# Performance work log

Measured on AMD Instinct MI355X. Metric: run time of the kernel, lower is better.

The kernel has to match this reference:

```python
import jax, jax.numpy as jnp
import numpy as np

N = 100000      # nodes
E = 1600000     # directed edges (before self-loops)
DIN = 128       # input feature dim
HID = 32        # per-head hidden dim
HEADS = 4
D1 = HID * HEADS  # 128, concat width
NG = 64         # graphs in batch
NEG_SLOPE = 0.2 # PyG GATConv leaky_relu slope


def setup_inputs() -> dict:
    key = jax.random.key(0)
    ks = jax.random.split(key, 16)
    s = 0.05
    x = jax.random.normal(ks[0], (N, DIN), dtype=jnp.float32)
    edge_index = jax.random.randint(ks[1], (2, E), 0, N, dtype=jnp.int32)
    batch = jnp.sort(jax.random.randint(ks[2], (N,), 0, NG, dtype=jnp.int32))
    # GATConv 1: in=DIN, out=HID, heads=HEADS, concat=True
    W1 = jax.random.normal(ks[3], (D1, DIN), dtype=jnp.float32) * s
    a1s = jax.random.normal(ks[4], (HEADS, HID), dtype=jnp.float32) * s
    a1d = jax.random.normal(ks[5], (HEADS, HID), dtype=jnp.float32) * s
    b1 = jnp.zeros((D1,), jnp.float32)
    # GATConv 2: in=D1, out=HID, heads=HEADS, concat=True
    W2 = jax.random.normal(ks[6], (D1, D1), dtype=jnp.float32) * s
    a2s = jax.random.normal(ks[7], (HEADS, HID), dtype=jnp.float32) * s
    a2d = jax.random.normal(ks[8], (HEADS, HID), dtype=jnp.float32) * s
    b2 = jnp.zeros((D1,), jnp.float32)
    # GATConv 3: in=D1, out=HID, heads=HEADS, concat=False (mean over heads)
    W3 = jax.random.normal(ks[9], (D1, D1), dtype=jnp.float32) * s
    a3s = jax.random.normal(ks[10], (HEADS, HID), dtype=jnp.float32) * s
    a3d = jax.random.normal(ks[11], (HEADS, HID), dtype=jnp.float32) * s
    b3 = jnp.zeros((HID,), jnp.float32)
    lin_w = jax.random.normal(ks[12], (1, HID), dtype=jnp.float32) * s
    lin_b = jnp.zeros((1,), jnp.float32)
    return {"x": x, "edge_index": edge_index, "batch": batch,
            "W1": W1, "a1s": a1s, "a1d": a1d, "b1": b1,
            "W2": W2, "a2s": a2s, "a2d": a2d, "b2": b2,
            "W3": W3, "a3s": a3s, "a3d": a3d, "b3": b3,
            "lin_w": lin_w, "lin_b": lin_b}


def _gat_conv(x, ei, W, att_src, att_dst, bias, concat):
    """PyG GATConv (no edge features, self-loops already in ei)."""
    n = x.shape[0]
    h = (x @ W.T).reshape(n, HEADS, HID)          # [N, H, C]
    src, dst = ei[0], ei[1]
    a_src = jnp.einsum('nhc,hc->nh', h, att_src)  # [N, H]
    a_dst = jnp.einsum('nhc,hc->nh', h, att_dst)
    e = jax.nn.leaky_relu(a_src[src] + a_dst[dst], NEG_SLOPE)  # [Etot, H]
    # segment softmax over incoming edges of each dst node
    e_max = jax.ops.segment_max(e, dst, num_segments=n)
    ex = jnp.exp(e - e_max[dst])
    denom = jax.ops.segment_sum(ex, dst, num_segments=n)
    alpha = ex / denom[dst]                        # [Etot, H]
    out = jax.ops.segment_sum(h[src] * alpha[:, :, None], dst, num_segments=n)
    if concat:
        out = out.reshape(n, HEADS * HID)
    else:
        out = out.mean(axis=1)
    return out + bias


def reference(x, edge_index, batch, W1, a1s, a1d, b1, W2, a2s, a2d, b2,
              W3, a3s, a3d, b3, lin_w, lin_b):
    loops = jnp.arange(N, dtype=edge_index.dtype)
    ei = jnp.concatenate([edge_index, jnp.stack([loops, loops])], axis=1)
    h = jax.nn.elu(_gat_conv(x, ei, W1, a1s, a1d, b1, True))
    h = jax.nn.elu(_gat_conv(h, ei, W2, a2s, a2d, b2, True))
    h = jax.nn.elu(_gat_conv(h, ei, W3, a3s, a3d, b3, False))
    h = h @ lin_w.T + lin_b                        # [N, 1]
    counts = jax.ops.segment_sum(jnp.ones((N,), h.dtype), batch, num_segments=NG)
    pooled = jax.ops.segment_sum(h, batch, num_segments=NG) / counts[:, None]
    return pooled.squeeze()                        # [NG]
```

## Files before the change

### kernel.cpp

```cpp
#include <hip/hip_runtime.h>
#include <hip/hip_fp16.h>
#include <math.h>

#define D1 128
#define NEG 0.2f
#define NODE_SHIFT 9
#define BIN_NODES 512
#define MAXBIN 256

typedef _Float16 v8h __attribute__((ext_vector_type(8)));
typedef float v4f __attribute__((ext_vector_type(4)));

__device__ __forceinline__ float lrelu(float v){ return v > 0.f ? v : NEG * v; }
__device__ __forceinline__ float elu_f(float v){ return v > 0.f ? v : __expf(v) - 1.f; }

__device__ __forceinline__ unsigned f2h2(float a, float b){
    return ((unsigned)__half_as_ushort(__float2half_rn(b)) << 16) |
           (unsigned)__half_as_ushort(__float2half_rn(a));
}
__device__ __forceinline__ float2 h2f2(unsigned u){
    float lo = __half2float(__ushort_as_half((unsigned short)(u & 0xffffu)));
    float hi = __half2float(__ushort_as_half((unsigned short)(u >> 16)));
    return make_float2(lo, hi);
}


__global__ __launch_bounds__(256) void kb_hist(const int* __restrict__ ei,
                                               int* __restrict__ binCnt,
                                               int n_edges, int etot, int nbin){
    __shared__ int h[MAXBIN];
    for (int i = threadIdx.x; i < nbin; i += 256) h[i] = 0;
    __syncthreads();
    int stride = gridDim.x * 256;
    for (int e = blockIdx.x * 256 + threadIdx.x; e < etot; e += stride){
        int dst = (e < n_edges) ? ei[n_edges + e] : (e - n_edges);
        atomicAdd(&h[dst >> NODE_SHIFT], 1);
    }
    __syncthreads();
    for (int i = threadIdx.x; i < nbin; i += 256)
        if (h[i]) atomicAdd(&binCnt[i], h[i]);
}

__global__ void kb_scan(const int* __restrict__ binCnt, int* __restrict__ binStart,
                        int* __restrict__ binCursor, int nbin,
                        int* __restrict__ rowptr, int n_nodes, int etot){
    if (threadIdx.x == 0){
        int run = 0;
        for (int b = 0; b < nbin; b++){
            binStart[b] = run; binCursor[b] = run; run += binCnt[b];
        }
        binStart[nbin] = run;
        rowptr[n_nodes] = etot;
    }
}

__global__ __launch_bounds__(256) void kb_scatter(const int* __restrict__ ei,
                                                  int* __restrict__ binCursor,
                                                  unsigned* __restrict__ staged,
                                                  int n_edges, int etot, int nbin){
    __shared__ int cnt[MAXBIN];
    __shared__ int base[MAXBIN];
    int e0 = blockIdx.x * 4096;
    for (int i = threadIdx.x; i < nbin; i += 256) cnt[i] = 0;
    __syncthreads();
    #pragma unroll 4
    for (int r = 0; r < 16; r++){
        int e = e0 + r * 256 + threadIdx.x;
        if (e < etot){
            int dst = (e < n_edges) ? ei[n_edges + e] : (e - n_edges);
            atomicAdd(&cnt[dst >> NODE_SHIFT], 1);
        }
    }
    __syncthreads();
    for (int i = threadIdx.x; i < nbin; i += 256){
        base[i] = cnt[i] ? atomicAdd(&binCursor[i], cnt[i]) : 0;
        cnt[i] = 0;
    }
    __syncthreads();
    #pragma unroll 4
    for (int r = 0; r < 16; r++){
        int e = e0 + r * 256 + threadIdx.x;
        if (e < etot){
            int src, dst;
            if (e < n_edges){ src = ei[e]; dst = ei[n_edges + e]; }
            else            { src = dst = e - n_edges; }
            int b = dst >> NODE_SHIFT;
            int p = base[b] + atomicAdd(&cnt[b], 1);
            staged[p] = ((unsigned)(dst & (BIN_NODES - 1)) << 17) | (unsigned)src;
        }
    }
}

__global__ __launch_bounds__(512) void kb_final(const unsigned* __restrict__ staged,
                                                const int* __restrict__ binStart,
                                                int* __restrict__ rowptr,
                                                int* __restrict__ eidx, int n_nodes){
    __shared__ int deg[BIN_NODES];
    __shared__ int cur[BIN_NODES];
    int b = blockIdx.x;
    int nbase = b << NODE_SHIFT;
    int s0 = binStart[b], s1 = binStart[b + 1];
    deg[threadIdx.x] = 0;
    __syncthreads();
    for (int i = s0 + threadIdx.x; i < s1; i += 512)
        atomicAdd(&deg[staged[i] >> 17], 1);
    __syncthreads();
    int v = deg[threadIdx.x];
    cur[threadIdx.x] = v;
    __syncthreads();
    for (int off = 1; off < BIN_NODES; off <<= 1){
        int t = (threadIdx.x >= off) ? cur[threadIdx.x - off] : 0;
        __syncthreads();
        cur[threadIdx.x] += t;
        __syncthreads();
    }
    int excl = cur[threadIdx.x] - v;
    int node = nbase + threadIdx.x;
    if (node < n_nodes) rowptr[node] = s0 + excl;
    cur[threadIdx.x] = s0 + excl;
    __syncthreads();
    for (int i = s0 + threadIdx.x; i < s1; i += 512){
        unsigned pr = staged[i];
        int p = atomicAdd(&cur[pr >> 17], 1);
        eidx[p] = (int)(pr & 0x1FFFFu);
    }
}


__global__ void k_prepw(const float* __restrict__ W1, const float* __restrict__ W2,
                        const float* __restrict__ W3, unsigned short* __restrict__ Bp){
    int t = blockIdx.x * 256 + threadIdx.x;
    if (t >= 49152) return;
    int w = t >> 14;
    int r = t & 16383;
    int k = r >> 7, j = r & 127;
    const float* W = (w == 0) ? W1 : (w == 1) ? W2 : W3;
    float val = W[j * 128 + k];
    int idx = (k >> 3) * 1024 + j * 8 + (k & 7);
    Bp[w * 16384 + idx] = __half_as_ushort(__float2half_rn(val));
}


template<int FP32SRC>
__global__ __launch_bounds__(256, 4) void k_mgemm(
        const float* __restrict__ Xf, const unsigned short* __restrict__ Xh,
        const unsigned short* __restrict__ Bp,
        const float* __restrict__ aw_s, const float* __restrict__ aw_d,
        unsigned short* __restrict__ Hh,
        float* __restrict__ asrc, float* __restrict__ adst, int n_rows){
    __shared__ unsigned short Bs[16384];
    int lane = threadIdx.x & 63;
    int wv   = threadIdx.x >> 6;
    int li = lane & 15, quad = lane >> 4;
    int r0 = blockIdx.x * 128 + wv * 32;

    int row0 = r0 + li;
    int row1 = r0 + 16 + li;
    int rc0 = row0 < n_rows ? row0 : 0;
    int rc1 = row1 < n_rows ? row1 : 0;

    v8h a0[4], a1[4];
    #pragma unroll
    for (int ks = 0; ks < 4; ks++){
        int koff = ks * 32 + quad * 8;
        if (FP32SRC){
            float f0[8], f1[8];
            *(float4*)&f0[0] = *(const float4*)(Xf + (size_t)rc0 * 128 + koff);
            *(float4*)&f0[4] = *(const float4*)(Xf + (size_t)rc0 * 128 + koff + 4);
            *(float4*)&f1[0] = *(const float4*)(Xf + (size_t)rc1 * 128 + koff);
            *(float4*)&f1[4] = *(const float4*)(Xf + (size_t)rc1 * 128 + koff + 4);
            #pragma unroll
            for (int i = 0; i < 8; i++){
                a0[ks][i] = (_Float16)f0[i];
                a1[ks][i] = (_Float16)f1[i];
            }
        } else {
            a0[ks] = *(const v8h*)(Xh + (size_t)rc0 * 128 + koff);
            a1[ks] = *(const v8h*)(Xh + (size_t)rc1 * 128 + koff);
        }
    }

    #pragma unroll
    for (int i = 0; i < 8; i++){
        int idx = threadIdx.x + i * 256;
        ((float4*)Bs)[idx] = ((const float4*)Bp)[idx];
    }
    __syncthreads();

    v4f acc[2][8];
    #pragma unroll
    for (int m = 0; m < 2; m++)
        #pragma unroll
        for (int t = 0; t < 8; t++)
            acc[m][t] = (v4f){0.f, 0.f, 0.f, 0.f};

    #pragma unroll
    for (int ks = 0; ks < 4; ks++){
        #pragma unroll
        for (int t = 0; t < 8; t++){
            int bo = (ks * 4 + quad) * 1024 + (t * 16 + li) * 8;
            v8h b = *(const v8h*)(Bs + bo);
            acc[0][t] = __builtin_amdgcn_mfma_f32_16x16x32_f16(a0[ks], b, acc[0][t], 0, 0, 0);
            acc[1][t] = __builtin_amdgcn_mfma_f32_16x16x32_f16(a1[ks], b, acc[1][t], 0, 0, 0);
        }
    }

    #pragma unroll
    for (int m = 0; m < 2; m++){
        #pragma unroll
        for (int t = 0; t < 8; t++){
            #pragma unroll
            for (int r = 0; r < 4; r++){
                float v  = acc[m][t][r];
                float vo = __shfl_xor(v, 1);
                if (!(li & 1)){
                    int row = r0 + m * 16 + quad * 4 + r;
                    if (row < n_rows)
                        *(unsigned*)(Hh + (size_t)row * 128 + t * 16 + li) = f2h2(v, vo);
                }
            }
        }
    }

    float as8[8], ad8[8];
    #pragma unroll
    for (int t = 0; t < 8; t++){
        as8[t] = aw_s[t * 16 + li];
        ad8[t] = aw_d[t * 16 + li];
    }
    #pragma unroll
    for (int m = 0; m < 2; m++){
        #pragma unroll
        for (int r = 0; r < 4; r++){
            float sp[4], dp[4];
            #pragma unroll
            for (int h = 0; h < 4; h++){
                sp[h] = acc[m][2*h][r] * as8[2*h] + acc[m][2*h+1][r] * as8[2*h+1];
                dp[h] = acc[m][2*h][r] * ad8[2*h] + acc[m][2*h+1][r] * ad8[2*h+1];
            }
            #pragma unroll
            for (int off = 1; off < 16; off <<= 1){
                #pragma unroll
                for (int h = 0; h < 4; h++){
                    sp[h] += __shfl_xor(sp[h], off);
                    dp[h] += __shfl_xor(dp[h], off);
                }
            }
            if (li == 0){
                int row = r0 + m * 16 + quad * 4 + r;
                if (row < n_rows){
                    ((float4*)asrc)[row] = make_float4(sp[0], sp[1], sp[2], sp[3]);
                    ((float4*)adst)[row] = make_float4(dp[0], dp[1], dp[2], dp[3]);
                }
            }
        }
    }
}


__device__ __forceinline__ void cons4(uint4 hv, float w, float* acc){
    unsigned u[4] = {hv.x, hv.y, hv.z, hv.w};
    #pragma unroll
    for (int q = 0; q < 4; q++){
        float2 f = h2f2(u[q]);
        acc[2*q]   = fmaf(w, f.x, acc[2*q]);
        acc[2*q+1] = fmaf(w, f.y, acc[2*q+1]);
    }
}

template<int MEAN>
__global__ __launch_bounds__(256, 8) void k_aggr(
        const unsigned* __restrict__ Hh,
        const float* __restrict__ asrc, const float* __restrict__ adst,
        const int* __restrict__ rowptr, const int* __restrict__ eidx,
        const float* __restrict__ bias,
        unsigned short* __restrict__ O, float* __restrict__ Of, int n_nodes){
    int lane = threadIdx.x & 63;
    int wid  = threadIdx.x >> 6;
    int n = __builtin_amdgcn_readfirstlane(blockIdx.x * 4 + wid);
    if (n >= n_nodes) return;
    int row0 = rowptr[n];
    int deg  = rowptr[n + 1] - row0;
    const int* ep = eidx + row0;
    int l  = lane;
    int eh = l & 3;
    int ej = l >> 2;
    int m  = l & 15;
    int wb = l & 60;
    int hb = l & 12;
    float4 ad = ((const float4*)adst)[n];
    float adw = eh == 0 ? ad.x : eh == 1 ? ad.y : eh == 2 ? ad.z : ad.w;

    const uint4* H4 = (const uint4*)Hh;
    float acc[8];
    #pragma unroll
    for (int q = 0; q < 8; q++) acc[q] = 0.f;
    float denp = 0.f;

    for (int i = 0; i < deg; i += 32){
        int rem = deg - i; if (rem > 32) rem = 32;
        int last = i + rem - 1;

        int j0 = i + ej;
        int sv0 = ep[j0 < last ? j0 : last];
        float t0 = asrc[(size_t)(unsigned)sv0 * 4u + (unsigned)eh] + adw;
        float w0f = __expf(fmaxf(t0, NEG * t0));
        float w0 = (ej < rem) ? w0f : 0.f;
        denp += w0;
        int w0i = __float_as_int(w0);

        int sv1 = sv0;
        int w1i = 0;
        if (rem > 16){
            int j1 = i + 16 + ej;
            sv1 = ep[j1 < last ? j1 : last];
            float t1 = asrc[(size_t)(unsigned)sv1 * 4u + (unsigned)eh] + adw;
            float w1f = __expf(fmaxf(t1, NEG * t1));
            float w1 = (16 + ej < rem) ? w1f : 0.f;
            denp += w1;
            w1i = __float_as_int(w1);
        }

        uint4 hv0, hv1, hv2, hv3, hv4, hv5, hv6, hv7;
#define GLOAD(t, svx) \
        if ((t) * 4 < rem){ \
            int s_ = __builtin_amdgcn_ds_bpermute((((t) & 3) << 6) + wb, svx); \
            hv##t = H4[(unsigned)s_ * 16u + (unsigned)m]; \
        }
#define GCONS(t, wxi) \
        if ((t) * 4 < rem){ \
            float wt_ = __int_as_float(__builtin_amdgcn_ds_bpermute((((t) & 3) << 6) + wb, wxi)); \
            cons4(hv##t, wt_, acc); \
        }
        GLOAD(0, sv0) GLOAD(1, sv0) GLOAD(2, sv0) GLOAD(3, sv0)
        GLOAD(4, sv1) GLOAD(5, sv1) GLOAD(6, sv1) GLOAD(7, sv1)
        GCONS(0, w0i) GCONS(1, w0i) GCONS(2, w0i) GCONS(3, w0i)
        GCONS(4, w1i) GCONS(5, w1i) GCONS(6, w1i) GCONS(7, w1i)
#undef GLOAD
#undef GCONS
    }

    #pragma unroll
    for (int q = 0; q < 8; q++){
        acc[q] += __shfl_xor(acc[q], 16);
        acc[q] += __shfl_xor(acc[q], 32);
    }
    denp += __shfl_xor(denp, 4);
    denp += __shfl_xor(denp, 8);
    denp += __shfl_xor(denp, 16);
    denp += __shfl_xor(denp, 32);
    float den = __int_as_float(__builtin_amdgcn_ds_bpermute(hb, __float_as_int(denp)));
    float rdh = 1.f / den;

    if (!MEAN){
        if (l < 16){
            float4 b0 = *(const float4*)(bias + m * 8);
            float4 b1 = *(const float4*)(bias + m * 8 + 4);
            float e0 = elu_f(acc[0] * rdh + b0.x);
            float e1 = elu_f(acc[1] * rdh + b0.y);
            float e2 = elu_f(acc[2] * rdh + b0.z);
            float e3 = elu_f(acc[3] * rdh + b0.w);
            float e4 = elu_f(acc[4] * rdh + b1.x);
            float e5 = elu_f(acc[5] * rdh + b1.y);
            float e6 = elu_f(acc[6] * rdh + b1.z);
            float e7 = elu_f(acc[7] * rdh + b1.w);
            uint4 ov;
            ov.x = f2h2(e0, e1); ov.y = f2h2(e2, e3);
            ov.z = f2h2(e4, e5); ov.w = f2h2(e6, e7);
            *(uint4*)(O + (size_t)n * 128 + m * 8) = ov;
        }
    } else {
        float v[8];
        #pragma unroll
        for (int q = 0; q < 8; q++) v[q] = acc[q] * rdh;
        #pragma unroll
        for (int q = 0; q < 8; q++){
            v[q] += __shfl_xor(v[q], 4);
            v[q] += __shfl_xor(v[q], 8);
        }
        if (l < 4){
            float4 o0, o1;
            o0.x = elu_f(v[0] * 0.25f + bias[l * 8 + 0]);
            o0.y = elu_f(v[1] * 0.25f + bias[l * 8 + 1]);
            o0.z = elu_f(v[2] * 0.25f + bias[l * 8 + 2]);
            o0.w = elu_f(v[3] * 0.25f + bias[l * 8 + 3]);
            o1.x = elu_f(v[4] * 0.25f + bias[l * 8 + 4]);
            o1.y = elu_f(v[5] * 0.25f + bias[l * 8 + 5]);
            o1.z = elu_f(v[6] * 0.25f + bias[l * 8 + 6]);
            o1.w = elu_f(v[7] * 0.25f + bias[l * 8 + 7]);
            *(float4*)(Of + (size_t)n * 32 + l * 8)     = o0;
            *(float4*)(Of + (size_t)n * 32 + l * 8 + 4) = o1;
        }
    }
}


__global__ void k_readout(const float* __restrict__ H3, const int* __restrict__ batch,
                          const float* __restrict__ lw, const float* __restrict__ lb,
                          float* __restrict__ pool, float* __restrict__ cnt, int n_nodes){
    __shared__ float pl[64];
    __shared__ float cl[64];
    if (threadIdx.x < 64){ pl[threadIdx.x] = 0.f; cl[threadIdx.x] = 0.f; }
    __syncthreads();
    int n = blockIdx.x * 256 + threadIdx.x;
    if (n < n_nodes){
        const float4* hp = (const float4*)(H3 + (size_t)n * 32);
        const float4* wp = (const float4*)lw;
        float y = 0.f;
        #pragma unroll
        for (int i = 0; i < 8; i++){
            float4 h4 = hp[i], w4 = wp[i];
            y += h4.x * w4.x + h4.y * w4.y + h4.z * w4.z + h4.w * w4.w;
        }
        y += lb[0];
        int b = batch[n];
        atomicAdd(&pl[b], y);
        atomicAdd(&cl[b], 1.f);
    }
    __syncthreads();
    if (threadIdx.x < 64 && cl[threadIdx.x] != 0.f){
        atomicAdd(&pool[threadIdx.x], pl[threadIdx.x]);
        atomicAdd(&cnt[threadIdx.x], cl[threadIdx.x]);
    }
}

__global__ void k_final(const float* __restrict__ pool, const float* __restrict__ cnt,
                        float* __restrict__ out){
    int g = threadIdx.x;
    if (g < 64) out[g] = (cnt[g] > 0.f) ? pool[g] / cnt[g] : 0.f;
}


extern "C" void kernel_launch(void* const* d_in, const int* in_sizes, int n_in,
                              void* d_out, int out_size, void* d_ws, size_t ws_size,
                              hipStream_t stream){
    const float* x   = (const float*)d_in[0];
    const int*   ei  = (const int*)  d_in[1];
    const int*   bat = (const int*)  d_in[2];
    const float* W1  = (const float*)d_in[3];
    const float* a1s = (const float*)d_in[4];
    const float* a1d = (const float*)d_in[5];
    const float* b1  = (const float*)d_in[6];
    const float* W2  = (const float*)d_in[7];
    const float* a2s = (const float*)d_in[8];
    const float* a2d = (const float*)d_in[9];
    const float* b2  = (const float*)d_in[10];
    const float* W3  = (const float*)d_in[11];
    const float* a3s = (const float*)d_in[12];
    const float* a3d = (const float*)d_in[13];
    const float* b3  = (const float*)d_in[14];
    const float* lw  = (const float*)d_in[15];
    const float* lb  = (const float*)d_in[16];
    (void)n_in; (void)out_size; (void)ws_size;

    const int n_nodes = in_sizes[0] / D1;
    const int n_edges = in_sizes[1] / 2;
    const int etot    = n_edges + n_nodes;
    const int nbin    = (n_nodes + BIN_NODES - 1) >> NODE_SHIFT;

    char* p = (char*)d_ws;
    size_t off = 0;
    auto alloc = [&](size_t bytes) -> char* {
        char* r = p + off;
        off = (off + bytes + 511) & ~(size_t)511;
        return r;
    };
    unsigned short* Hh   = (unsigned short*)alloc((size_t)n_nodes * 128 * 2);
    unsigned short* Xh   = (unsigned short*)alloc((size_t)n_nodes * 128 * 2);
    float*          asrc = (float*)alloc((size_t)n_nodes * 4 * 4);
    float*          adst = (float*)alloc((size_t)n_nodes * 4 * 4);
    unsigned short* Bp   = (unsigned short*)alloc(3 * 16384 * 2);
    int*      rowptr  = (int*)alloc((size_t)(n_nodes + 1) * 4);
    int*      eidx    = (int*)alloc((size_t)etot * 4);
    unsigned* staged  = (unsigned*)alloc((size_t)etot * 4);
    int*      binCnt  = (int*)alloc(MAXBIN * 4);
    int*      binStart= (int*)alloc((MAXBIN + 1) * 4);
    int*      binCur  = (int*)alloc(MAXBIN * 4);
    float*    pool    = (float*)alloc(64 * 4);
    float*    cnt     = (float*)alloc(64 * 4);
    float*    h3      = (float*)Xh;

    hipMemsetAsync(binCnt, 0, MAXBIN * 4, stream);
    hipMemsetAsync(pool, 0, 64 * 4, stream);
    hipMemsetAsync(cnt, 0, 64 * 4, stream);

    k_prepw<<<192, 256, 0, stream>>>(W1, W2, W3, Bp);

    int cb = (etot + 4095) / 4096;
    kb_hist<<<cb, 256, 0, stream>>>(ei, binCnt, n_edges, etot, nbin);
    kb_scan<<<1, 64, 0, stream>>>(binCnt, binStart, binCur, nbin, rowptr, n_nodes, etot);
    kb_scatter<<<cb, 256, 0, stream>>>(ei, binCur, staged, n_edges, etot, nbin);
    kb_final<<<nbin, 512, 0, stream>>>(staged, binStart, rowptr, eidx, n_nodes);

    int mb = (n_nodes + 127) / 128;
    int rb = (n_nodes + 3) / 4;

    k_mgemm<1><<<mb, 256, 0, stream>>>(x, nullptr, Bp,
                                       a1s, a1d, Hh, asrc, adst, n_nodes);
    k_aggr<0><<<rb, 256, 0, stream>>>((const unsigned*)Hh, asrc, adst, rowptr, eidx,
                                      b1, Xh, nullptr, n_nodes);
    k_mgemm<0><<<mb, 256, 0, stream>>>(nullptr, Xh, Bp + 16384,
                                       a2s, a2d, Hh, asrc, adst, n_nodes);
    k_aggr<0><<<rb, 256, 0, stream>>>((const unsigned*)Hh, asrc, adst, rowptr, eidx,
                                      b2, Xh, nullptr, n_nodes);
    k_mgemm<0><<<mb, 256, 0, stream>>>(nullptr, Xh, Bp + 32768,
                                       a3s, a3d, Hh, asrc, adst, n_nodes);
    k_aggr<1><<<rb, 256, 0, stream>>>((const unsigned*)Hh, asrc, adst, rowptr, eidx,
                                      b3, nullptr, h3, n_nodes);

    int ob = (n_nodes + 255) / 256;
    k_readout<<<ob, 256, 0, stream>>>(h3, bat, lw, lb, pool, cnt, n_nodes);
    k_final<<<1, 64, 0, stream>>>(pool, cnt, (float*)d_out);
}
```

Measured before the change: 479.6 us.

## Fuse readout into final aggregation and use fma_mix for fp16 accumulate

The final-layer aggregation kernel now computes the linear readout and pools per-graph sums directly, using 64 slotted global atomics per graph to spread contention, and the separate readout kernel and h3 buffer are removed. The edge accumulation loop also uses inline v_fma_mix_f32 to fuse the fp16-to-fp32 conversion with the FMA. This removes one kernel launch and the round trip of the layer-3 activations, and it cuts ALU work in the hot gather loop. In exchange there are many more global atomics, one per node, and the inline assembly ties the code to the target ISA.

```diff
diff --git a/kernel.cpp b/kernel.cpp
--- a/kernel.cpp
+++ b/kernel.cpp
@@ -11,17 +11,11 @@
 typedef _Float16 v8h __attribute__((ext_vector_type(8)));
 typedef float v4f __attribute__((ext_vector_type(4)));
 
-__device__ __forceinline__ float lrelu(float v){ return v > 0.f ? v : NEG * v; }
 __device__ __forceinline__ float elu_f(float v){ return v > 0.f ? v : __expf(v) - 1.f; }
 
 __device__ __forceinline__ unsigned f2h2(float a, float b){
     return ((unsigned)__half_as_ushort(__float2half_rn(b)) << 16) |
            (unsigned)__half_as_ushort(__float2half_rn(a));
-}
-__device__ __forceinline__ float2 h2f2(unsigned u){
-    float lo = __half2float(__ushort_as_half((unsigned short)(u & 0xffffu)));
-    float hi = __half2float(__ushort_as_half((unsigned short)(u >> 16)));
-    return make_float2(lo, hi);
 }
 
 
@@ -262,9 +256,10 @@
     unsigned u[4] = {hv.x, hv.y, hv.z, hv.w};
     #pragma unroll
     for (int q = 0; q < 4; q++){
-        float2 f = h2f2(u[q]);
-        acc[2*q]   = fmaf(w, f.x, acc[2*q]);
-        acc[2*q+1] = fmaf(w, f.y, acc[2*q+1]);
+        asm("v_fma_mix_f32 %0, %1, %2, %0 op_sel:[0,0,0] op_sel_hi:[1,0,0]"
+            : "+v"(acc[2*q])     : "v"(u[q]), "v"(w));
+        asm("v_fma_mix_f32 %0, %1, %2, %0 op_sel:[1,0,0] op_sel_hi:[1,0,0]"
+            : "+v"(acc[2*q+1])   : "v"(u[q]), "v"(w));
     }
 }
 
@@ -274,7 +269,10 @@
         const float* __restrict__ asrc, const float* __restrict__ adst,
         const int* __restrict__ rowptr, const int* __restrict__ eidx,
         const float* __restrict__ bias,
-        unsigned short* __restrict__ O, float* __restrict__ Of, int n_nodes){
+        unsigned short* __restrict__ O,
+        const int* __restrict__ batch, const float* __restrict__ lw,
+        const float* __restrict__ lb,
+        float* __restrict__ pool2, float* __restrict__ cnt2, int n_nodes){
     int lane = threadIdx.x & 63;
     int wid  = threadIdx.x >> 6;
     int n = __builtin_amdgcn_readfirstlane(blockIdx.x * 4 + wid);
@@ -378,56 +376,44 @@
             v[q] += __shfl_xor(v[q], 4);
             v[q] += __shfl_xor(v[q], 8);
         }
+        float part = 0.f;
         if (l < 4){
-            float4 o0, o1;
-            o0.x = elu_f(v[0] * 0.25f + bias[l * 8 + 0]);
-            o0.y = elu_f(v[1] * 0.25f + bias[l * 8 + 1]);
-            o0.z = elu_f(v[2] * 0.25f + bias[l * 8 + 2]);
-            o0.w = elu_f(v[3] * 0.25f + bias[l * 8 + 3]);
-            o1.x = elu_f(v[4] * 0.25f + bias[l * 8 + 4]);
-            o1.y = elu_f(v[5] * 0.25f + bias[l * 8 + 5]);
-            o1.z = elu_f(v[6] * 0.25f + bias[l * 8 + 6]);
-            o1.w = elu_f(v[7] * 0.25f + bias[l * 8 + 7]);
-            *(float4*)(Of + (size_t)n * 32 + l * 8)     = o0;
-            *(float4*)(Of + (size_t)n * 32 + l * 8 + 4) = o1;
-        }
-    }
-}
-
-
-__global__ void k_readout(const float* __restrict__ H3, const int* __restrict__ batch,
-                          const float* __restrict__ lw, const float* __restrict__ lb,
-                          float* __restrict__ pool, float* __restrict__ cnt, int n_nodes){
-    __shared__ float pl[64];
-    __shared__ float cl[64];
-    if (threadIdx.x < 64){ pl[threadIdx.x] = 0.f; cl[threadIdx.x] = 0.f; }
-    __syncthreads();
-    int n = blockIdx.x * 256 + threadIdx.x;
-    if (n < n_nodes){
-        const float4* hp = (const float4*)(H3 + (size_t)n * 32);
-        const float4* wp = (const float4*)lw;
-        float y = 0.f;
-        #pragma unroll
-        for (int i = 0; i < 8; i++){
-            float4 h4 = hp[i], w4 = wp[i];
-            y += h4.x * w4.x + h4.y * w4.y + h4.z * w4.z + h4.w * w4.w;
-        }
-        y += lb[0];
-        int b = batch[n];
-        atomicAdd(&pl[b], y);
-        atomicAdd(&cl[b], 1.f);
-    }
-    __syncthreads();
-    if (threadIdx.x < 64 && cl[threadIdx.x] != 0.f){
-        atomicAdd(&pool[threadIdx.x], pl[threadIdx.x]);
-        atomicAdd(&cnt[threadIdx.x], cl[threadIdx.x]);
-    }
-}
-
-__global__ void k_final(const float* __restrict__ pool, const float* __restrict__ cnt,
+            float4 w0 = *(const float4*)(lw + l * 8);
+            float4 w1 = *(const float4*)(lw + l * 8 + 4);
+            float e0 = elu_f(v[0] * 0.25f + bias[l * 8 + 0]);
+            float e1 = elu_f(v[1] * 0.25f + bias[l * 8 + 1]);
+            float e2 = elu_f(v[2] * 0.25f + bias[l * 8 + 2]);
+            float e3 = elu_f(v[3] * 0.25f + bias[l * 8 + 3]);
+            float e4 = elu_f(v[4] * 0.25f + bias[l * 8 + 4]);
+            float e5 = elu_f(v[5] * 0.25f + bias[l * 8 + 5]);
+            float e6 = elu_f(v[6] * 0.25f + bias[l * 8 + 6]);
+            float e7 = elu_f(v[7] * 0.25f + bias[l * 8 + 7]);
+            part = e0 * w0.x + e1 * w0.y + e2 * w0.z + e3 * w0.w
+                 + e4 * w1.x + e5 * w1.y + e6 * w1.z + e7 * w1.w;
+        }
+        part += __shfl_xor(part, 1);
+        part += __shfl_xor(part, 2);
+        if (l == 0){
+            int b = batch[n];
+            int slot = (int)(blockIdx.x & 63);
+            atomicAdd(&pool2[b * 64 + slot], part + lb[0]);
+            atomicAdd(&cnt2[b * 64 + slot], 1.f);
+        }
+    }
+}
+
+
+__global__ void k_final(const float* __restrict__ pool2, const float* __restrict__ cnt2,
                         float* __restrict__ out){
     int g = threadIdx.x;
-    if (g < 64) out[g] = (cnt[g] > 0.f) ? pool[g] / cnt[g] : 0.f;
+    if (g < 64){
+        float ps = 0.f, cs = 0.f;
+        for (int s = 0; s < 64; s++){
+            ps += pool2[g * 64 + s];
+            cs += cnt2[g * 64 + s];
+        }
+        out[g] = (cs > 0.f) ? ps / cs : 0.f;
+    }
 }
 
 
@@ -476,13 +462,12 @@
     int*      binCnt  = (int*)alloc(MAXBIN * 4);
     int*      binStart= (int*)alloc((MAXBIN + 1) * 4);
     int*      binCur  = (int*)alloc(MAXBIN * 4);
-    float*    pool    = (float*)alloc(64 * 4);
-    float*    cnt     = (float*)alloc(64 * 4);
-    float*    h3      = (float*)Xh;
+    float*    pool2   = (float*)alloc(64 * 64 * 4);
+    float*    cnt2    = (float*)alloc(64 * 64 * 4);
 
     hipMemsetAsync(binCnt, 0, MAXBIN * 4, stream);
-    hipMemsetAsync(pool, 0, 64 * 4, stream);
-    hipMemsetAsync(cnt, 0, 64 * 4, stream);
+    hipMemsetAsync(pool2, 0, 64 * 64 * 4, stream);
+    hipMemsetAsync(cnt2, 0, 64 * 64 * 4, stream);
 
     k_prepw<<<192, 256, 0, stream>>>(W1, W2, W3, Bp);
 
@@ -498,17 +483,18 @@
     k_mgemm<1><<<mb, 256, 0, stream>>>(x, nullptr, Bp,
                                        a1s, a1d, Hh, asrc, adst, n_nodes);
     k_aggr<0><<<rb, 256, 0, stream>>>((const unsigned*)Hh, asrc, adst, rowptr, eidx,
-                                      b1, Xh, nullptr, n_nodes);
+                                      b1, Xh, nullptr, nullptr, nullptr,
+                                      nullptr, nullptr, n_nodes);
     k_mgemm<0><<<mb, 256, 0, stream>>>(nullptr, Xh, Bp + 16384,
                                        a2s, a2d, Hh, asrc, adst, n_nodes);
     k_aggr<0><<<rb, 256, 0, stream>>>((const unsigned*)Hh, asrc, adst, rowptr, eidx,
-                                      b2, Xh, nullptr, n_nodes);
+                                      b2, Xh, nullptr, nullptr, nullptr,
+                                      nullptr, nullptr, n_nodes);
     k_mgemm<0><<<mb, 256, 0, stream>>>(nullptr, Xh, Bp + 32768,
                                        a3s, a3d, Hh, asrc, adst, n_nodes);
     k_aggr<1><<<rb, 256, 0, stream>>>((const unsigned*)Hh, asrc, adst, rowptr, eidx,
-                                      b3, nullptr, h3, n_nodes);
-
-    int ob = (n_nodes + 255) / 256;
-    k_readout<<<ob, 256, 0, stream>>>(h3, bat, lw, lb, pool, cnt, n_nodes);
-    k_final<<<1, 64, 0, stream>>>(pool, cnt, (float*)d_out);
-}
+                                      b3, nullptr, bat, lw, lb,
+                                      pool2, cnt2, n_nodes);
+
+    k_final<<<1, 64, 0, stream>>>(pool2, cnt2, (float*)d_out);
+}
```

New measurement: 499.1 us. +4.1%, slower.
